# Performance work log

Hardware: AMD Instinct MI355X
Metric: run time of the kernel (lower is better)

The kernel has to match this reference:

```python
import jax, jax.numpy as jnp
import numpy as np

N, IN_F, OUT_F = 8192, 512, 256
NEG_INF = -9e15
LEAKY_SLOPE = 0.25


def setup_inputs() -> dict:
    key = jax.random.key(0)
    k1, k2, k3, k4, k5, k6 = jax.random.split(key, 6)
    inp = {
        "input": jax.random.normal(k1, (N, IN_F), dtype=jnp.float32),
        "adj": jax.random.randint(k2, (N, N), 0, 2, dtype=jnp.int32),
        # learned params (xavier-normal-ish scale)
        "weights": jax.random.normal(k3, (IN_F, OUT_F), dtype=jnp.float32) * (2.0 / (IN_F + OUT_F)) ** 0.5,
        "a1": jax.random.normal(k4, (OUT_F, 1), dtype=jnp.float32) * (2.0 / (OUT_F + 1)) ** 0.5,
        "a2": jax.random.normal(k5, (OUT_F, 1), dtype=jnp.float32) * (2.0 / (OUT_F + 1)) ** 0.5,
        "bias": jax.random.uniform(k6, (OUT_F,), dtype=jnp.float32, minval=-1.0 / OUT_F ** 0.5, maxval=1.0 / OUT_F ** 0.5),
    }
    return inp


def reference(input, adj, weights, a1, a2, bias):
    # h = input @ W  : [N, out]
    h = input @ weights
    # e[i,j] = leaky_relu((h@a1)[i] + (h@a2)[j])  : [N, N] via broadcast
    e1 = h @ a1  # [N,1]
    e2 = h @ a2  # [N,1]
    e = e1 + e2.T
    e = jnp.where(e > 0, e, LEAKY_SLOPE * e)
    # mask non-edges, row softmax (dropout omitted: deterministic reference)
    scores = jnp.where(adj > 0, e, NEG_INF)
    attention = jax.nn.softmax(scores, axis=1)
    # aggregate + bias
    return attention @ h + bias
```

## Files before the change

kernel.cpp:

```cpp
#include <hip/hip_runtime.h>

typedef __attribute__((ext_vector_type(8))) short short8;
typedef __attribute__((ext_vector_type(4))) float floatx4;
typedef __attribute__((ext_vector_type(4))) unsigned int uintx4;
typedef __attribute__((ext_vector_type(2))) unsigned int uintx2;
typedef __attribute__((ext_vector_type(4))) int intx4;
typedef __attribute__((ext_vector_type(4))) unsigned short ushortx4;
typedef unsigned int u32;

#define NN 8192
#define KIN 512
#define COUT 256
#define SHIFT 16.0f

#define AS1 __attribute__((address_space(1)))
#define AS3 __attribute__((address_space(3)))

__device__ __forceinline__ void stage16(const void* g, void* l) {
  __builtin_amdgcn_global_load_lds((const AS1 u32*)g, (AS3 u32*)l, 16, 0, 0);
}

__device__ __forceinline__ unsigned int f2bf(float f) {
  unsigned int u = __float_as_uint(f);
  return (u + 0x7FFFu + ((u >> 16) & 1u)) >> 16;
}

__device__ __forceinline__ u32 pkbf(float lo, float hi) {
  u32 a = __float_as_uint(lo) + 0x8000u;
  u32 b = __float_as_uint(hi) + 0x8000u;
  return __builtin_amdgcn_perm(b, a, 0x07060302u);
}

__device__ __forceinline__ short8 pack8(const float* p) {
  uintx4 w;
  w.x = pkbf(p[0], p[1]);
  w.y = pkbf(p[2], p[3]);
  w.z = pkbf(p[4], p[5]);
  w.w = pkbf(p[6], p[7]);
  union { uintx4 u; short8 s; } cv; cv.u = w;
  return cv.s;
}

__global__ void k_cast_input(const float* __restrict__ in, ushortx4* __restrict__ out) {
  int idx = blockIdx.x * 256 + threadIdx.x;
  floatx4 v = ((const floatx4*)in)[idx];
  ushortx4 o;
  o.x = (unsigned short)f2bf(v.x);
  o.y = (unsigned short)f2bf(v.y);
  o.z = (unsigned short)f2bf(v.z);
  o.w = (unsigned short)f2bf(v.w);
  out[idx] = o;
}

__global__ void k_prep_w(const float* __restrict__ w, unsigned short* __restrict__ wt) {
  int idx = blockIdx.x * 256 + threadIdx.x;
  int k = idx >> 8, c = idx & 255;
  wt[c * KIN + k] = (unsigned short)f2bf(w[idx]);
}

__global__ __launch_bounds__(256)
void k_gemm_h(const unsigned short* __restrict__ inA, const unsigned short* __restrict__ wt,
              const float* __restrict__ a1, const float* __restrict__ a2,
              unsigned short* __restrict__ ht, float* __restrict__ e1, float* __restrict__ e2,
              float* __restrict__ A1, float* __restrict__ A2, u32* __restrict__ e2pk) {
  int wave = threadIdx.x >> 6;
  int lane = threadIdx.x & 63;
  int n = lane & 15, q = lane >> 4;
  int row0 = blockIdx.x * 64 + wave * 16;
  int mrow = row0 + n;

  floatx4 acc[16];
#pragma unroll
  for (int t = 0; t < 16; ++t) acc[t] = (floatx4){0.f, 0.f, 0.f, 0.f};

  for (int kc = 0; kc < KIN / 32; ++kc) {
    int k0 = kc * 32 + q * 8;
    short8 a = *(const short8*)(inA + (size_t)mrow * KIN + k0);
#pragma unroll
    for (int nt = 0; nt < 16; ++nt) {
      short8 b = *(const short8*)(wt + (size_t)(nt * 16 + n) * KIN + k0);
      acc[nt] = __builtin_amdgcn_mfma_f32_16x16x32_bf16(a, b, acc[nt], 0, 0, 0);
    }
  }

  int i0 = row0 + q * 4;
#pragma unroll
  for (int nt = 0; nt < 16; ++nt) {
    int c = nt * 16 + n;
    uintx2 pk;
    pk.x = f2bf(acc[nt][0]) | (f2bf(acc[nt][1]) << 16);
    pk.y = f2bf(acc[nt][2]) | (f2bf(acc[nt][3]) << 16);
    *(uintx2*)(ht + (size_t)c * NN + i0) = pk;
  }

  float s1[4] = {0.f, 0.f, 0.f, 0.f}, s2[4] = {0.f, 0.f, 0.f, 0.f};
#pragma unroll
  for (int nt = 0; nt < 16; ++nt) {
    float w1 = a1[nt * 16 + n];
    float w2 = a2[nt * 16 + n];
#pragma unroll
    for (int r = 0; r < 4; ++r) {
      s1[r] += acc[nt][r] * w1;
      s2[r] += acc[nt][r] * w2;
    }
  }
#pragma unroll
  for (int m = 1; m < 16; m <<= 1) {
#pragma unroll
    for (int r = 0; r < 4; ++r) {
      s1[r] += __shfl_xor(s1[r], m);
      s2[r] += __shfl_xor(s2[r], m);
    }
  }
  if (n == 0) {
#pragma unroll
    for (int r = 0; r < 4; ++r) {
      float v1 = s1[r], v2 = s2[r];
      e1[i0 + r] = v1;
      e2[i0 + r] = v2;
      A1[i0 + r] = __expf(v1 - 8.0f);
      A2[i0 + r] = __expf(0.25f * v1 - 8.0f);
      u32 b1 = f2bf(__expf(v2 - 8.0f));
      u32 b2 = f2bf(__expf(0.25f * v2 - 8.0f));
      e2pk[i0 + r] = (b1 << 16) | b2;
    }
  }
}

__global__ __launch_bounds__(256, 2)
void k_attn_fused(const int* __restrict__ adj, const unsigned short* __restrict__ ht,
                  const float* __restrict__ A1, const float* __restrict__ A2,
                  const u32* __restrict__ e2pk,
                  float* __restrict__ opart, float* __restrict__ Dpart) {
  __shared__ __align__(16) char smem[69632];
  u32* e2s = (u32*)(smem + 65536);

  int b = blockIdx.x;
  int rg = b >> 3, js = b & 7;
  int wave = threadIdx.x >> 6, lane = threadIdx.x & 63;
  int n = lane & 15, q = lane >> 4;
  int rowblock = rg * 128;
  int rowbase = rowblock + wave * 32;
  int jbeg = js * 1024;

  ((uintx4*)e2s)[threadIdx.x] = *(const uintx4*)(e2pk + jbeg + threadIdx.x * 4);

  float A1v0 = A1[rowbase + n],      A2v0 = A2[rowbase + n];
  float A1v1 = A1[rowbase + 16 + n], A2v1 = A2[rowbase + 16 + n];

  floatx4 acc[2][16];
  floatx4 accd[2];
#pragma unroll
  for (int t = 0; t < 2; ++t) {
    accd[t] = (floatx4){0.f, 0.f, 0.f, 0.f};
#pragma unroll
    for (int nt = 0; nt < 16; ++nt) acc[t][nt] = (floatx4){0.f, 0.f, 0.f, 0.f};
  }

  union { uintx4 u; short8 s; } onesu;
  onesu.u = (uintx4){0x3F803F80u, 0x3F803F80u, 0x3F803F80u, 0x3F803F80u};
  short8 ones = onesu.s;

  auto stage = [&](int ch, int buf) {
    int j0g = jbeg + ch * 32;
    char* hbase = smem + buf * 32768;
#pragma unroll
    for (int i = 0; i < 4; ++i) {
      int seg = wave * 256 + i * 64 + lane;
      int c = seg >> 2;
      int j8 = (seg & 3) * 8;
      stage16(ht + (size_t)c * NN + j0g + j8, hbase + (size_t)(wave * 256 + i * 64) * 16);
    }
    char* abase = hbase + 16384 + wave * 4096;
    const int* aw = adj + (size_t)(rowblock + wave * 32) * NN + j0g;
#pragma unroll
    for (int i = 0; i < 4; ++i) {
      stage16(aw + (size_t)(i * 8 + (lane & 7)) * NN + (lane >> 3) * 4, abase + i * 1024);
    }
  };

  int rlo = n & 7, rhi = n >> 3;

  stage(0, 0);
  asm volatile("s_waitcnt lgkmcnt(0)" ::: "memory");
  asm volatile("s_barrier" ::: "memory");

  for (int ch = 0; ch < 32; ++ch) {
    int cur = ch & 1;
    if (ch < 31) {
      stage(ch + 1, cur ^ 1);
      asm volatile("s_waitcnt vmcnt(8)" ::: "memory");
    } else {
      asm volatile("s_waitcnt vmcnt(0)" ::: "memory");
    }

    const char* ab = smem + cur * 32768 + 16384 + wave * 4096;
    intx4 a0a = *(const intx4*)(ab + rhi * 1024 + q * 256 + rlo * 16);
    intx4 a0b = *(const intx4*)(ab + rhi * 1024 + q * 256 + 128 + rlo * 16);
    intx4 a1a = *(const intx4*)(ab + 2048 + rhi * 1024 + q * 256 + rlo * 16);
    intx4 a1b = *(const intx4*)(ab + 2048 + rhi * 1024 + q * 256 + 128 + rlo * 16);

    uintx4 ba = *(const uintx4*)(e2s + ch * 32 + q * 8);
    uintx4 bb = *(const uintx4*)(e2s + ch * 32 + q * 8 + 4);
    u32 bw[8] = {ba.x, ba.y, ba.z, ba.w, bb.x, bb.y, bb.z, bb.w};

    float p0[8], p1[8];
#pragma unroll
    for (int jj = 0; jj < 8; ++jj) {
      int av0 = (jj < 4) ? a0a[jj] : a0b[jj - 4];
      int av1 = (jj < 4) ? a1a[jj] : a1b[jj - 4];
      float B1 = __uint_as_float(bw[jj] & 0xffff0000u);
      float B2 = __uint_as_float(bw[jj] << 16);
      float m10 = A1v0 * B1, m20 = A2v0 * B2;
      float m11 = A1v1 * B1, m21 = A2v1 * B2;
      float pm0 = fmaxf(m10, m20);
      float pm1 = fmaxf(m11, m21);
      p0[jj] = (av0 != 0) ? pm0 : 0.f;
      p1[jj] = (av1 != 0) ? pm1 : 0.f;
    }
    short8 af0 = pack8(p0);
    short8 af1 = pack8(p1);

    asm volatile("s_barrier" ::: "memory");

    const short8* lb = (const short8*)(smem + (size_t)cur * 32768);
#pragma unroll
    for (int t = 0; t < 16; ++t) {
      short8 bf = lb[t * 64 + n * 4 + q];
      acc[0][t] = __builtin_amdgcn_mfma_f32_16x16x32_bf16(af0, bf, acc[0][t], 0, 0, 0);
      acc[1][t] = __builtin_amdgcn_mfma_f32_16x16x32_bf16(af1, bf, acc[1][t], 0, 0, 0);
    }
    accd[0] = __builtin_amdgcn_mfma_f32_16x16x32_bf16(af0, ones, accd[0], 0, 0, 0);
    accd[1] = __builtin_amdgcn_mfma_f32_16x16x32_bf16(af1, ones, accd[1], 0, 0, 0);

    asm volatile("s_waitcnt lgkmcnt(0)" ::: "memory");
    asm volatile("s_barrier" ::: "memory");
  }

  if (n == 0) {
#pragma unroll
    for (int t2 = 0; t2 < 2; ++t2)
#pragma unroll
      for (int r = 0; r < 4; ++r)
        Dpart[(size_t)js * NN + rowbase + t2 * 16 + q * 4 + r] = accd[t2][r];
  }

  float* op = opart + (size_t)js * NN * COUT;
#pragma unroll
  for (int t2 = 0; t2 < 2; ++t2) {
#pragma unroll
    for (int nt = 0; nt < 16; ++nt) {
#pragma unroll
      for (int r = 0; r < 4; ++r) {
        int i = rowbase + t2 * 16 + q * 4 + r;
        op[(size_t)i * COUT + nt * 16 + n] = acc[t2][nt][r];
      }
    }
  }
}

__global__ void k_final_part(float* __restrict__ out, const float* __restrict__ opart,
                             const float* __restrict__ Dpart, const float* __restrict__ bias) {
  int i = blockIdx.x;
  int c = threadIdx.x;
  float s = 0.f, d = 0.f;
#pragma unroll
  for (int js = 0; js < 8; ++js) {
    s += opart[((size_t)js * NN + i) * COUT + c];
    d += Dpart[(size_t)js * NN + i];
  }
  out[(size_t)i * COUT + c] = s / fmaxf(d, 1e-37f) + bias[c];
}

__global__ __launch_bounds__(256, 2)
void k_attn_atomic(const int* __restrict__ adj, const unsigned short* __restrict__ ht,
                   const float* __restrict__ e1, const float* __restrict__ e2,
                   float* __restrict__ out_num, float* __restrict__ Dbuf) {
  int b = blockIdx.x;
  int rg = b >> 3, js = b & 7;
  int wave = threadIdx.x >> 6, lane = threadIdx.x & 63;
  int n = lane & 15, q = lane >> 4;
  int rowbase = rg * 128 + wave * 32;

  float e1v0 = e1[rowbase + n];
  float e1v1 = e1[rowbase + 16 + n];

  floatx4 acc[2][16];
#pragma unroll
  for (int t = 0; t < 2; ++t)
#pragma unroll
    for (int nt = 0; nt < 16; ++nt) acc[t][nt] = (floatx4){0.f, 0.f, 0.f, 0.f};

  float d0 = 0.f, d1 = 0.f;
  int jbeg = js * 1024;

  for (int ch = 0; ch < 32; ++ch) {
    int j0 = jbeg + ch * 32 + q * 8;
    floatx4 ea = *(const floatx4*)(e2 + j0);
    floatx4 eb = *(const floatx4*)(e2 + j0 + 4);
    float ev[8] = {ea.x, ea.y, ea.z, ea.w, eb.x, eb.y, eb.z, eb.w};

    intx4 A00 = *(const intx4*)(adj + (size_t)(rowbase + n) * NN + j0);
    intx4 A01 = *(const intx4*)(adj + (size_t)(rowbase + n) * NN + j0 + 4);
    intx4 A10 = *(const intx4*)(adj + (size_t)(rowbase + 16 + n) * NN + j0);
    intx4 A11 = *(const intx4*)(adj + (size_t)(rowbase + 16 + n) * NN + j0 + 4);

    float p0[8], p1[8];
#pragma unroll
    for (int jj = 0; jj < 8; ++jj) {
      int av0 = (jj < 4) ? A00[jj] : A01[jj - 4];
      int av1 = (jj < 4) ? A10[jj] : A11[jj - 4];
      float t0 = e1v0 + ev[jj];
      float t1 = e1v1 + ev[jj];
      float f0 = fmaxf(t0, 0.25f * t0);
      float f1 = fmaxf(t1, 0.25f * t1);
      float x0 = __expf(f0 - SHIFT);
      float x1 = __expf(f1 - SHIFT);
      p0[jj] = (av0 != 0) ? x0 : 0.f;
      p1[jj] = (av1 != 0) ? x1 : 0.f;
      d0 += p0[jj];
      d1 += p1[jj];
    }
    short8 af0 = pack8(p0);
    short8 af1 = pack8(p1);

#pragma unroll
    for (int g = 0; g < 2; ++g) {
      short8 bf[8];
#pragma unroll
      for (int t = 0; t < 8; ++t)
        bf[t] = *(const short8*)(ht + (size_t)((g * 8 + t) * 16 + n) * NN + j0);
#pragma unroll
      for (int t = 0; t < 8; ++t) {
        acc[0][g * 8 + t] = __builtin_amdgcn_mfma_f32_16x16x32_bf16(af0, bf[t], acc[0][g * 8 + t], 0, 0, 0);
        acc[1][g * 8 + t] = __builtin_amdgcn_mfma_f32_16x16x32_bf16(af1, bf[t], acc[1][g * 8 + t], 0, 0, 0);
      }
    }
  }

  d0 += __shfl_xor(d0, 16); d0 += __shfl_xor(d0, 32);
  d1 += __shfl_xor(d1, 16); d1 += __shfl_xor(d1, 32);
  if (lane < 16) {
    atomicAdd(Dbuf + rowbase + lane, d0);
    atomicAdd(Dbuf + rowbase + 16 + lane, d1);
  }

#pragma unroll
  for (int t2 = 0; t2 < 2; ++t2) {
#pragma unroll
    for (int nt = 0; nt < 16; ++nt) {
#pragma unroll
      for (int r = 0; r < 4; ++r) {
        int i = rowbase + t2 * 16 + q * 4 + r;
        atomicAdd(out_num + (size_t)i * COUT + nt * 16 + n, acc[t2][nt][r]);
      }
    }
  }
}

__global__ void k_final_atomic(float* __restrict__ out, const float* __restrict__ Dbuf,
                               const float* __restrict__ bias) {
  int idx = blockIdx.x * 256 + threadIdx.x;
  int i = idx >> 8, c = idx & 255;
  float d = fmaxf(Dbuf[i], 1e-37f);
  out[idx] = out[idx] / d + bias[c];
}

extern "C" void kernel_launch(void* const* d_in, const int* in_sizes, int n_in,
                              void* d_out, int out_size, void* d_ws, size_t ws_size,
                              hipStream_t stream) {
  const float* input   = (const float*)d_in[0];
  const int*   adj     = (const int*)d_in[1];
  const float* weights = (const float*)d_in[2];
  const float* a1      = (const float*)d_in[3];
  const float* a2      = (const float*)d_in[4];
  const float* bias    = (const float*)d_in[5];
  float* out = (float*)d_out;
  char* ws = (char*)d_ws;

  unsigned short* inA = (unsigned short*)(ws);
  unsigned short* wt  = (unsigned short*)(ws + 8388608);
  unsigned short* ht  = (unsigned short*)(ws + 8650752);
  float* e1    = (float*)(ws + 12845056);
  float* e2    = (float*)(ws + 12877824);
  float* A1    = (float*)(ws + 12910592);
  float* A2    = (float*)(ws + 12943360);
  u32*   e2pk  = (u32*)  (ws + 12976128);
  float* Dpart = (float*)(ws + 13008896);
  float* opart = (float*)(ws + 13271040);
  const size_t WS_NEEDED_PART = 13271040 + (size_t)8 * NN * COUT * 4;
  float* Dbuf = Dpart;

  k_cast_input<<<4096, 256, 0, stream>>>(input, (ushortx4*)inA);
  k_prep_w<<<512, 256, 0, stream>>>(weights, wt);
  k_gemm_h<<<128, 256, 0, stream>>>(inA, wt, a1, a2, ht, e1, e2, A1, A2, e2pk);

  if (ws_size >= WS_NEEDED_PART) {
    k_attn_fused<<<512, 256, 0, stream>>>(adj, ht, A1, A2, e2pk, opart, Dpart);
    k_final_part<<<8192, 256, 0, stream>>>(out, opart, Dpart, bias);
  } else {
    hipMemsetAsync(out, 0, (size_t)NN * COUT * sizeof(float), stream);
    hipMemsetAsync(Dbuf, 0, NN * sizeof(float), stream);
    k_attn_atomic<<<512, 256, 0, stream>>>(adj, ht, e1, e2, out, Dbuf);
    k_final_atomic<<<8192, 256, 0, stream>>>(out, Dbuf, bias);
  }
}
```

Before: 455.6 us.

## Fuse input cast into GEMM and store split partial outputs as fp16

Removes the separate input-to-bf16 cast kernel by converting fp32 input rows to bf16 inside the projection GEMM. Stores the per-split attention partial numerators as packed half2 instead of fp32, halving the intermediate buffer written by the attention kernel and read by the final reduction. This trades lower memory traffic and one fewer launch for reduced precision in the unnormalized partial sums, with some risk of accuracy loss or overflow in fp16.

```diff
diff --git a/kernel.cpp b/kernel.cpp
--- a/kernel.cpp
+++ b/kernel.cpp
@@ -1,4 +1,5 @@
 #include <hip/hip_runtime.h>
+#include <hip/hip_fp16.h>
 
 typedef __attribute__((ext_vector_type(8))) short short8;
 typedef __attribute__((ext_vector_type(4))) float floatx4;
@@ -41,17 +42,6 @@
   return cv.s;
 }
 
-__global__ void k_cast_input(const float* __restrict__ in, ushortx4* __restrict__ out) {
-  int idx = blockIdx.x * 256 + threadIdx.x;
-  floatx4 v = ((const floatx4*)in)[idx];
-  ushortx4 o;
-  o.x = (unsigned short)f2bf(v.x);
-  o.y = (unsigned short)f2bf(v.y);
-  o.z = (unsigned short)f2bf(v.z);
-  o.w = (unsigned short)f2bf(v.w);
-  out[idx] = o;
-}
-
 __global__ void k_prep_w(const float* __restrict__ w, unsigned short* __restrict__ wt) {
   int idx = blockIdx.x * 256 + threadIdx.x;
   int k = idx >> 8, c = idx & 255;
@@ -59,7 +49,7 @@
 }
 
 __global__ __launch_bounds__(256)
-void k_gemm_h(const unsigned short* __restrict__ inA, const unsigned short* __restrict__ wt,
+void k_gemm_h(const float* __restrict__ input, const unsigned short* __restrict__ wt,
               const float* __restrict__ a1, const float* __restrict__ a2,
               unsigned short* __restrict__ ht, float* __restrict__ e1, float* __restrict__ e2,
               float* __restrict__ A1, float* __restrict__ A2, u32* __restrict__ e2pk) {
@@ -75,7 +65,15 @@
 
   for (int kc = 0; kc < KIN / 32; ++kc) {
     int k0 = kc * 32 + q * 8;
-    short8 a = *(const short8*)(inA + (size_t)mrow * KIN + k0);
+    const float* ip = input + (size_t)mrow * KIN + k0;
+    floatx4 va = *(const floatx4*)(ip);
+    floatx4 vb = *(const floatx4*)(ip + 4);
+    union { uintx4 u; short8 s; } av;
+    av.u.x = f2bf(va.x) | (f2bf(va.y) << 16);
+    av.u.y = f2bf(va.z) | (f2bf(va.w) << 16);
+    av.u.z = f2bf(vb.x) | (f2bf(vb.y) << 16);
+    av.u.w = f2bf(vb.z) | (f2bf(vb.w) << 16);
+    short8 a = av.s;
 #pragma unroll
     for (int nt = 0; nt < 16; ++nt) {
       short8 b = *(const short8*)(wt + (size_t)(nt * 16 + n) * KIN + k0);
@@ -131,7 +129,7 @@
 void k_attn_fused(const int* __restrict__ adj, const unsigned short* __restrict__ ht,
                   const float* __restrict__ A1, const float* __restrict__ A2,
                   const u32* __restrict__ e2pk,
-                  float* __restrict__ opart, float* __restrict__ Dpart) {
+                  __half2* __restrict__ oph, float* __restrict__ Dpart) {
   __shared__ __align__(16) char smem[69632];
   u32* e2s = (u32*)(smem + 65536);
 
@@ -245,28 +243,30 @@
         Dpart[(size_t)js * NN + rowbase + t2 * 16 + q * 4 + r] = accd[t2][r];
   }
 
-  float* op = opart + (size_t)js * NN * COUT;
 #pragma unroll
   for (int t2 = 0; t2 < 2; ++t2) {
+    int ibase = rowbase + t2 * 16 + q * 4;
 #pragma unroll
     for (int nt = 0; nt < 16; ++nt) {
-#pragma unroll
-      for (int r = 0; r < 4; ++r) {
-        int i = rowbase + t2 * 16 + q * 4 + r;
-        op[(size_t)i * COUT + nt * 16 + n] = acc[t2][nt][r];
-      }
-    }
-  }
-}
-
-__global__ void k_final_part(float* __restrict__ out, const float* __restrict__ opart,
+      int c = nt * 16 + n;
+      oph[((size_t)js * 4096 + (ibase >> 1)) * 256 + c] =
+          __floats2half2_rn(acc[t2][nt][0], acc[t2][nt][1]);
+      oph[((size_t)js * 4096 + (ibase >> 1) + 1) * 256 + c] =
+          __floats2half2_rn(acc[t2][nt][2], acc[t2][nt][3]);
+    }
+  }
+}
+
+__global__ void k_final_part(float* __restrict__ out, const __half2* __restrict__ oph,
                              const float* __restrict__ Dpart, const float* __restrict__ bias) {
   int i = blockIdx.x;
   int c = threadIdx.x;
+  int hi = i & 1;
   float s = 0.f, d = 0.f;
 #pragma unroll
   for (int js = 0; js < 8; ++js) {
-    s += opart[((size_t)js * NN + i) * COUT + c];
+    __half2 h2 = oph[((size_t)js * 4096 + (i >> 1)) * 256 + c];
+    s += hi ? __high2float(h2) : __low2float(h2);
     d += Dpart[(size_t)js * NN + i];
   }
   out[(size_t)i * COUT + c] = s / fmaxf(d, 1e-37f) + bias[c];
@@ -378,7 +378,6 @@
   float* out = (float*)d_out;
   char* ws = (char*)d_ws;
 
-  unsigned short* inA = (unsigned short*)(ws);
   unsigned short* wt  = (unsigned short*)(ws + 8388608);
   unsigned short* ht  = (unsigned short*)(ws + 8650752);
   float* e1    = (float*)(ws + 12845056);
@@ -387,17 +386,16 @@
   float* A2    = (float*)(ws + 12943360);
   u32*   e2pk  = (u32*)  (ws + 12976128);
   float* Dpart = (float*)(ws + 13008896);
-  float* opart = (float*)(ws + 13271040);
-  const size_t WS_NEEDED_PART = 13271040 + (size_t)8 * NN * COUT * 4;
+  __half2* oph = (__half2*)(ws + 13271040);
+  const size_t WS_NEEDED_PART = 13271040 + (size_t)8 * NN * COUT * 2;
   float* Dbuf = Dpart;
 
-  k_cast_input<<<4096, 256, 0, stream>>>(input, (ushortx4*)inA);
   k_prep_w<<<512, 256, 0, stream>>>(weights, wt);
-  k_gemm_h<<<128, 256, 0, stream>>>(inA, wt, a1, a2, ht, e1, e2, A1, A2, e2pk);
+  k_gemm_h<<<128, 256, 0, stream>>>(input, wt, a1, a2, ht, e1, e2, A1, A2, e2pk);
 
   if (ws_size >= WS_NEEDED_PART) {
-    k_attn_fused<<<512, 256, 0, stream>>>(adj, ht, A1, A2, e2pk, opart, Dpart);
-    k_final_part<<<8192, 256, 0, stream>>>(out, opart, Dpart, bias);
+    k_attn_fused<<<512, 256, 0, stream>>>(adj, ht, A1, A2, e2pk, oph, Dpart);
+    k_final_part<<<8192, 256, 0, stream>>>(out, oph, Dpart, bias);
   } else {
     hipMemsetAsync(out, 0, (size_t)NN * COUT * sizeof(float), stream);
     hipMemsetAsync(Dbuf, 0, NN * sizeof(float), stream);
```

After: 476.3 us. +4.5%, slower.
